# Optimization experiments

Hardware: AMD Instinct MI355X
Metric: run time of the kernel (lower is better)

Reference implementation:

```python
import jax, jax.numpy as jnp
import numpy as np

N_BUS = 4096
BATCH = 1024


def setup_inputs() -> dict:
    key = jax.random.key(0)
    ks = jax.random.split(key, 10)
    u = jax.random.normal(ks[0], (BATCH, N_BUS), dtype=jnp.float32)
    w = jax.random.normal(ks[1], (BATCH, N_BUS), dtype=jnp.float32)
    # parameters (torch.rand -> uniform[0,1); Linear init ~ U(-1/sqrt(n), 1/sqrt(n)))
    G = jax.random.uniform(ks[2], (N_BUS, N_BUS), dtype=jnp.float32)
    B = jax.random.uniform(ks[3], (N_BUS, N_BUS), dtype=jnp.float32)
    bias_p = jax.random.uniform(ks[4], (1, N_BUS), dtype=jnp.float32)
    bias_q = jax.random.uniform(ks[5], (1, N_BUS), dtype=jnp.float32)
    lim = 1.0 / np.sqrt(N_BUS)
    Wp = jax.random.uniform(ks[6], (N_BUS, N_BUS), dtype=jnp.float32, minval=-lim, maxval=lim)
    bp = jax.random.uniform(ks[7], (N_BUS,), dtype=jnp.float32, minval=-lim, maxval=lim)
    Wq = jax.random.uniform(ks[8], (N_BUS, N_BUS), dtype=jnp.float32, minval=-lim, maxval=lim)
    bq = jax.random.uniform(ks[9], (N_BUS,), dtype=jnp.float32, minval=-lim, maxval=lim)
    return {"u": u, "w": w, "G": G, "B": B, "bias_p": bias_p, "bias_q": bias_q,
            "Wp": Wp, "bp": bp, "Wq": Wq, "bq": bq}


def reference(u, w, G, B, bias_p, bias_q, Wp, bp, Wq, bq):
    # Algebraically identical to the original's outer-product form:
    # p_i = sum_k (u_i u_k + w_i w_k) G_ik + (w_i u_k - u_i w_k) B_ik
    #     = u_i (G u)_i + w_i (G w)_i + w_i (B u)_i - u_i (B w)_i
    # q_i = sum_k (w_i u_k - u_i w_k) G_ik - (u_i u_k + w_i w_k) B_ik
    #     = w_i (G u)_i - u_i (G w)_i - u_i (B u)_i - w_i (B w)_i
    Gu = u @ G.T  # (batch, n_bus): (G u)_i = sum_k G_ik u_k
    Gw = w @ G.T
    Bu = u @ B.T
    Bw = w @ B.T
    p = u * Gu + w * Gw + w * Bu - u * Bw + bias_p
    q = w * Gu - u * Gw - u * Bu - w * Bw + bias_q
    # nn.Linear: y = x @ W^T + b
    p = p @ Wp.T + bp
    q = q @ Wq.T + bq
    return (p, q)
```

## Files before the change

kernel.cpp:

```cpp
#include <hip/hip_runtime.h>
#include <hip/hip_bf16.h>

#define NB 4096
#define MB 1024
#define SZ ((size_t)MB * NB)
#define NN ((size_t)NB * NB)

typedef __bf16 bf16_t;
typedef __attribute__((ext_vector_type(8))) __bf16 bf16x8;
typedef __attribute__((ext_vector_type(4))) float f32x4;
typedef __attribute__((ext_vector_type(4))) unsigned int u32x4;

#define AS1 __attribute__((address_space(1)))
#define AS3 __attribute__((address_space(3)))
#define GLOAD16(gp, lp)                                                        \
  __builtin_amdgcn_global_load_lds((const AS1 unsigned int*)(gp),              \
                                   (AS3 unsigned int*)(lp), 16, 0, 0)
#define SBAR() __builtin_amdgcn_s_barrier()
#define SCHEDB() __builtin_amdgcn_sched_barrier(0)
#define MFMA16(a, b, c) __builtin_amdgcn_mfma_f32_16x16x32_bf16((a), (b), (c), 0, 0, 0)
#define VMCNT4() asm volatile("s_waitcnt vmcnt(4)" ::: "memory")
#define VMCNT0() asm volatile("s_waitcnt vmcnt(0)" ::: "memory")

__device__ __forceinline__ bf16x8 neg8(bf16x8 x) {
  u32x4 t;
  __builtin_memcpy(&t, &x, 16);
  t ^= 0x80008000u;
  bf16x8 y;
  __builtin_memcpy(&y, &t, 16);
  return y;
}

__device__ __forceinline__ bf16x8 cvt8(float4 a, float4 b) {
  bf16x8 v;
  v[0] = (bf16_t)a.x; v[1] = (bf16_t)a.y; v[2] = (bf16_t)a.z; v[3] = (bf16_t)a.w;
  v[4] = (bf16_t)b.x; v[5] = (bf16_t)b.y; v[6] = (bf16_t)b.z; v[7] = (bf16_t)b.w;
  return v;
}

#define ITEM_S (SZ / 8)
#define ITEM_N (NN / 8)

__global__ __launch_bounds__(256) void prep6_kernel(
    const float* __restrict__ u, const float* __restrict__ w,
    const float* __restrict__ G, const float* __restrict__ Bm,
    const float* __restrict__ Wp, const float* __restrict__ Wq,
    bf16_t* __restrict__ ws) {
  size_t stride = (size_t)gridDim.x * blockDim.x;
  const size_t tot = 2 * ITEM_S + 4 * ITEM_N;
  for (size_t i = (size_t)blockIdx.x * blockDim.x + threadIdx.x; i < tot;
       i += stride) {
    const float* src;
    bf16_t* dst;
    size_t off;
    if (i < ITEM_S) { src = u; dst = ws; off = i; }
    else if (i < 2 * ITEM_S) { src = w; dst = ws + SZ; off = i - ITEM_S; }
    else if (i < 2 * ITEM_S + ITEM_N) { src = G; dst = ws + 2 * SZ; off = i - 2 * ITEM_S; }
    else if (i < 2 * ITEM_S + 2 * ITEM_N) { src = Bm; dst = ws + 2 * SZ + NN; off = i - 2 * ITEM_S - ITEM_N; }
    else if (i < 2 * ITEM_S + 3 * ITEM_N) { src = Wp; dst = ws + 2 * SZ + 2 * NN; off = i - 2 * ITEM_S - 2 * ITEM_N; }
    else { src = Wq; dst = ws + 2 * SZ + 3 * NN; off = i - 2 * ITEM_S - 3 * ITEM_N; }
    const float4* s = reinterpret_cast<const float4*>(src) + off * 2;
    reinterpret_cast<bf16x8*>(dst)[off] = cvt8(s[0], s[1]);
  }
}

__global__ __launch_bounds__(256) void prep4_kernel(
    const float* __restrict__ u, const float* __restrict__ w,
    const float* __restrict__ G, const float* __restrict__ Bm,
    bf16_t* __restrict__ ws) {
  size_t stride = (size_t)gridDim.x * blockDim.x;
  const size_t tot = 2 * ITEM_S + 2 * ITEM_N;
  for (size_t i = (size_t)blockIdx.x * blockDim.x + threadIdx.x; i < tot;
       i += stride) {
    const float* src;
    bf16_t* dst;
    size_t off;
    if (i < ITEM_S) { src = u; dst = ws; off = i; }
    else if (i < 2 * ITEM_S) { src = w; dst = ws + SZ; off = i - ITEM_S; }
    else if (i < 2 * ITEM_S + ITEM_N) { src = G; dst = ws + 2 * SZ; off = i - 2 * ITEM_S; }
    else { src = Bm; dst = ws + 2 * SZ + NN; off = i - 2 * ITEM_S - ITEM_N; }
    const float4* s = reinterpret_cast<const float4*>(src) + off * 2;
    reinterpret_cast<bf16x8*>(dst)[off] = cvt8(s[0], s[1]);
  }
}

__global__ __launch_bounds__(512, 2) void fused1_v3(
    const float* __restrict__ u, const float* __restrict__ w,
    const bf16_t* __restrict__ ubf, const bf16_t* __restrict__ wbf,
    const bf16_t* __restrict__ Gbf, const bf16_t* __restrict__ Bbf,
    const float* __restrict__ bias_p, const float* __restrict__ bias_q,
    bf16_t* __restrict__ pq) {
  __shared__ bf16_t lds[2][4][128 * 64];
  const int tid = threadIdx.x, lane = tid & 63, wv = tid >> 6;
  const int bid = blockIdx.x;
  const int t = (bid & 7) * 32 + (bid >> 3);
  const int row0 = (t & 7) * 128, col0 = (t >> 3) * 128;
  const int wm = (wv >> 2) * 64, wn = (wv & 3) * 32;
  const int lr = lane & 15, kq = lane >> 4;

  const int rA = tid >> 3;
  const int kkc = (tid & 7) ^ (rA & 7);
  const bf16_t* bases[4] = {ubf, wbf, Gbf, Bbf};
  const int r0s[4] = {row0, row0, col0, col0};
  const bf16_t* gsA[4];
  const bf16_t* gsB[4];
#pragma unroll
  for (int o = 0; o < 4; ++o) {
    gsA[o] = bases[o] + (size_t)(r0s[o] + rA) * NB + kkc * 8;
    gsB[o] = gsA[o] + (size_t)64 * NB;
  }

#define F1_ST(bufv, o, ktn)                                                    \
  do {                                                                         \
    GLOAD16(gsA[o] + (ktn), &lds[bufv][o][wv * 512]);                          \
    GLOAD16(gsB[o] + (ktn), &lds[bufv][o][4096 + wv * 512]);                   \
  } while (0)

  int kread[2], aoff[4], boff[2];
#pragma unroll
  for (int ks = 0; ks < 2; ++ks) kread[ks] = ((ks * 4 + kq) ^ (lr & 7)) << 3;
#pragma unroll
  for (int m = 0; m < 4; ++m) aoff[m] = (wm + m * 16 + lr) * 64;
#pragma unroll
  for (int n = 0; n < 2; ++n) boff[n] = (wn + n * 16 + lr) * 64;

#define F1_LD(o, roff, ks) \
  (*reinterpret_cast<const bf16x8*>(&lds[cur][o][(roff) + kread[ks]]))

  f32x4 aS[4][2] = {}, aT[4][2] = {};

  {
    F1_ST(0, 0, 0); F1_ST(0, 1, 0); F1_ST(0, 2, 0); F1_ST(0, 3, 0);
    VMCNT0();
  }
  __syncthreads();

  const int NIT = NB / 64;
  for (int it = 0; it < NIT; ++it) {
    const int cur = it & 1;
    const int nxt = cur ^ 1;
    const bool pf = (it + 1) < NIT;
    const int ktn = (it + 1) * 64;
#pragma unroll
    for (int ks = 0; ks < 2; ++ks) {
      bf16x8 bG[2], bB[2], bBn[2];
#pragma unroll
      for (int mh = 0; mh < 2; ++mh) {
        if (mh == 0) {
          bG[0] = F1_LD(2, boff[0], ks);
          bG[1] = F1_LD(2, boff[1], ks);
          bB[0] = F1_LD(3, boff[0], ks);
          bB[1] = F1_LD(3, boff[1], ks);
          bBn[0] = neg8(bB[0]);
          bBn[1] = neg8(bB[1]);
        }
        bf16x8 au2[2], aw2[2];
#pragma unroll
        for (int i = 0; i < 2; ++i) {
          au2[i] = F1_LD(0, aoff[2 * mh + i], ks);
          aw2[i] = F1_LD(1, aoff[2 * mh + i], ks);
        }
        if (ks == 0 && pf) {
          if (mh == 0) { F1_ST(nxt, 0, ktn); F1_ST(nxt, 1, ktn); }
          else         { F1_ST(nxt, 2, ktn); F1_ST(nxt, 3, ktn); }
        }
        SBAR();
        SCHEDB();
        __builtin_amdgcn_s_setprio(1);
#pragma unroll
        for (int i = 0; i < 2; ++i) {
          const int m = 2 * mh + i;
#pragma unroll
          for (int n = 0; n < 2; ++n) {
            aS[m][n] = MFMA16(au2[i], bG[n], aS[m][n]);
            aS[m][n] = MFMA16(aw2[i], bBn[n], aS[m][n]);
            aT[m][n] = MFMA16(aw2[i], bG[n], aT[m][n]);
            aT[m][n] = MFMA16(au2[i], bB[n], aT[m][n]);
          }
        }
        __builtin_amdgcn_s_setprio(0);
        SCHEDB();
        if (ks == 1 && mh == 1) VMCNT0();
        SBAR();
        SCHEDB();
      }
    }
  }

  const int fr = lane & 15, fq = kq;
#pragma unroll
  for (int m = 0; m < 4; ++m)
#pragma unroll
    for (int n = 0; n < 2; ++n)
#pragma unroll
      for (int j = 0; j < 4; ++j) {
        int r = row0 + wm + m * 16 + fq * 4 + j;
        int c = col0 + wn + n * 16 + fr;
        size_t idx = (size_t)r * NB + c;
        float U = u[idx], W = w[idx];
        float S = aS[m][n][j], T = aT[m][n][j];
        pq[idx] = (bf16_t)(U * S + W * T + bias_p[c]);
        pq[SZ + idx] = (bf16_t)(W * S - U * T + bias_q[c]);
      }
}

__global__ __launch_bounds__(256, 2) void gemm2_v9(
    const bf16_t* __restrict__ pq, const bf16_t* __restrict__ Wpb,
    const bf16_t* __restrict__ Wqb, const float* __restrict__ bp,
    const float* __restrict__ bq, float* __restrict__ out) {
  __shared__ bf16_t lds[4][2][128 * 32];
  const int tid = threadIdx.x, lane = tid & 63, wv = tid >> 6;
  const int bid = blockIdx.x;
  const int t = (bid & 7) * 64 + (bid >> 3);
  const int z = t >> 8;
  const int s = t & 255;
  const int row0 = (s & 7) * 128, col0 = (s >> 3) * 128;

  const bf16_t* A = pq + (size_t)z * SZ;
  const bf16_t* Wm = z ? Wqb : Wpb;
  const float* bias = z ? bq : bp;
  float* C = out + (size_t)z * SZ;

  const int wm = (wv >> 1) * 64, wn = (wv & 1) * 64;
  const int lr = lane & 15, kq = lane >> 4;
  const int kswz = (kq ^ ((lr >> 1) & 3)) << 3;

  const int srow = tid >> 2;
  const int sc = (tid & 3) ^ ((tid >> 3) & 3);
  const bf16_t* gA0 = A + (size_t)(row0 + srow) * NB + sc * 8;
  const bf16_t* gA1 = gA0 + (size_t)64 * NB;
  const bf16_t* gW0 = Wm + (size_t)(col0 + srow) * NB + sc * 8;
  const bf16_t* gW1 = gW0 + (size_t)64 * NB;

#define G2_ISSUE(hh)                                                           \
  do {                                                                         \
    const int _sl = (hh) & 3;                                                  \
    const int _ko = (hh) * 32;                                                 \
    GLOAD16(gA0 + _ko, &lds[_sl][0][wv * 512]);                                \
    GLOAD16(gA1 + _ko, &lds[_sl][0][2048 + wv * 512]);                         \
    GLOAD16(gW0 + _ko, &lds[_sl][1][wv * 512]);                                \
    GLOAD16(gW1 + _ko, &lds[_sl][1][2048 + wv * 512]);                         \
  } while (0)

  int aoff[4], woff[4];
#pragma unroll
  for (int m = 0; m < 4; ++m) aoff[m] = (wm + m * 16 + lr) * 32 + kswz;
#pragma unroll
  for (int n = 0; n < 4; ++n) woff[n] = (wn + n * 16 + lr) * 32 + kswz;

  f32x4 acc[4][4] = {};

  G2_ISSUE(0); G2_ISSUE(1); G2_ISSUE(2);
  VMCNT4();
  SBAR();
  SCHEDB();

  const int HTOT = 2 * (NB / 64);
  for (int h = 0; h < HTOT; ++h) {
    const int slot = h & 3;
    const bool pf = (h + 3) < HTOT;

    bf16x8 av[4], bw[4];
#pragma unroll
    for (int m = 0; m < 4; ++m)
      av[m] = *reinterpret_cast<const bf16x8*>(&lds[slot][0][aoff[m]]);
#pragma unroll
    for (int n = 0; n < 4; ++n)
      bw[n] = *reinterpret_cast<const bf16x8*>(&lds[slot][1][woff[n]]);
    if (pf) G2_ISSUE(h + 3);
#pragma unroll
    for (int m = 0; m < 4; ++m)
#pragma unroll
      for (int n = 0; n < 4; ++n)
        acc[m][n] = MFMA16(av[m], bw[n], acc[m][n]);
    if (h < HTOT - 3)
      VMCNT4();
    else if (h == HTOT - 3)
      asm volatile("s_waitcnt vmcnt(2)" ::: "memory");
    else if (h == HTOT - 2)
      VMCNT0();
    SBAR();
    SCHEDB();
  }

  const int fr = lane & 15, fq = kq;
#pragma unroll
  for (int m = 0; m < 4; ++m)
#pragma unroll
    for (int n = 0; n < 4; ++n)
#pragma unroll
      for (int j = 0; j < 4; ++j) {
        int r = row0 + wm + m * 16 + fq * 4 + j;
        int c = col0 + wn + n * 16 + fr;
        C[(size_t)r * NB + c] = acc[m][n][j] + bias[c];
      }
}

__device__ __forceinline__ int swz_off32(int r, int kk) {
  return r * 32 + ((kk ^ ((r >> 1) & 3)) << 3);
}

__device__ __forceinline__ void fb_stage_f32(const float* __restrict__ src,
                                             int row0, int k0, bf16_t* lds, int t) {
  int r = t >> 2, kk = t & 3;
  const float* p = src + (size_t)(row0 + r) * NB + k0 + (kk << 3);
  float4 v0 = *reinterpret_cast<const float4*>(p);
  float4 v1 = *reinterpret_cast<const float4*>(p + 4);
  *reinterpret_cast<bf16x8*>(lds + swz_off32(r, kk)) = cvt8(v0, v1);
}

__global__ __launch_bounds__(256, 2) void fb_gemm2(
    const bf16_t* __restrict__ pq, const float* __restrict__ Wp,
    const float* __restrict__ Wq, const float* __restrict__ bp,
    const float* __restrict__ bq, float* __restrict__ out) {
  __shared__ bf16_t lA[128 * 32], lW[128 * 32];
  const int z = blockIdx.z;
  const bf16_t* A = pq + (size_t)z * SZ;
  const float* Wm = z ? Wq : Wp;
  const float* bias = z ? bq : bp;
  float* C = out + (size_t)z * SZ;
  const int tid = threadIdx.x;
  const int lane = tid & 63, wv = tid >> 6;
  const int wm = (wv >> 1) * 64, wn = (wv & 1) * 64;
  const int row0 = blockIdx.y * 128, col0 = blockIdx.x * 128;
  const int lr = lane & 15, kq = lane >> 4;
  const int fslot = (kq ^ ((lr >> 1) & 3)) << 3;
  f32x4 acc[4][4] = {};
  for (int kt = 0; kt < NB; kt += 32) {
#pragma unroll
    for (int p = 0; p < 2; ++p) {
      int cb = p * 256 + wv * 64;
      int ci = cb + lane;
      int r = ci >> 2, kl = ci & 3;
      int ks = kl ^ ((r >> 1) & 3);
      const bf16_t* g = A + (size_t)(row0 + r) * NB + kt + (ks << 3);
      GLOAD16(g, lA + cb * 8);
    }
#pragma unroll
    for (int p = 0; p < 2; ++p)
      fb_stage_f32(Wm, col0, kt, lW, p * 256 + tid);
    __syncthreads();
    bf16x8 af[4], bg[4];
#pragma unroll
    for (int m = 0; m < 4; ++m)
      af[m] = *reinterpret_cast<const bf16x8*>(lA + (wm + m * 16 + lr) * 32 + fslot);
#pragma unroll
    for (int n = 0; n < 4; ++n)
      bg[n] = *reinterpret_cast<const bf16x8*>(lW + (wn + n * 16 + lr) * 32 + fslot);
#pragma unroll
    for (int m = 0; m < 4; ++m)
#pragma unroll
      for (int n = 0; n < 4; ++n)
        acc[m][n] = MFMA16(af[m], bg[n], acc[m][n]);
    __syncthreads();
  }
  const int fr = lane & 15, fq = lane >> 4;
#pragma unroll
  for (int m = 0; m < 4; ++m)
#pragma unroll
    for (int n = 0; n < 4; ++n)
#pragma unroll
      for (int j = 0; j < 4; ++j) {
        int r = row0 + wm + m * 16 + fq * 4 + j;
        int c = col0 + wn + n * 16 + fr;
        C[(size_t)r * NB + c] = acc[m][n][j] + bias[c];
      }
}

__global__ __launch_bounds__(512, 2) void fb_fused1(
    const float* __restrict__ u, const float* __restrict__ w,
    const float* __restrict__ G, const float* __restrict__ Bm,
    const float* __restrict__ bias_p, const float* __restrict__ bias_q,
    bf16_t* __restrict__ pq) {
  __shared__ bf16_t lU[128 * 32], lW[128 * 32], lG[128 * 32], lB[128 * 32];
  const int tid = threadIdx.x;
  const int lane = tid & 63, wv = tid >> 6;
  const int wm = (wv >> 2) * 64, wn = (wv & 3) * 32;
  const int row0 = blockIdx.y * 128, col0 = blockIdx.x * 128;
  const int lr = lane & 15, kq = lane >> 4;
  const int fslot = (kq ^ ((lr >> 1) & 3)) << 3;
  f32x4 aS[4][2] = {}, aT[4][2] = {};
  for (int kt = 0; kt < NB; kt += 32) {
    fb_stage_f32(u, row0, kt, lU, tid);
    fb_stage_f32(w, row0, kt, lW, tid);
    fb_stage_f32(G, col0, kt, lG, tid);
    fb_stage_f32(Bm, col0, kt, lB, tid);
    __syncthreads();
    bf16x8 au[4], aw[4], bG[2], bB[2], bBn[2];
#pragma unroll
    for (int m = 0; m < 4; ++m) {
      int off = (wm + m * 16 + lr) * 32 + fslot;
      au[m] = *reinterpret_cast<const bf16x8*>(lU + off);
      aw[m] = *reinterpret_cast<const bf16x8*>(lW + off);
    }
#pragma unroll
    for (int n = 0; n < 2; ++n) {
      int off = (wn + n * 16 + lr) * 32 + fslot;
      bG[n] = *reinterpret_cast<const bf16x8*>(lG + off);
      bB[n] = *reinterpret_cast<const bf16x8*>(lB + off);
      bBn[n] = neg8(bB[n]);
    }
#pragma unroll
    for (int m = 0; m < 4; ++m)
#pragma unroll
      for (int n = 0; n < 2; ++n) {
        aS[m][n] = MFMA16(au[m], bG[n], aS[m][n]);
        aS[m][n] = MFMA16(aw[m], bBn[n], aS[m][n]);
        aT[m][n] = MFMA16(aw[m], bG[n], aT[m][n]);
        aT[m][n] = MFMA16(au[m], bB[n], aT[m][n]);
      }
    __syncthreads();
  }
  const int fr = lane & 15, fq = lane >> 4;
#pragma unroll
  for (int m = 0; m < 4; ++m)
#pragma unroll
    for (int n = 0; n < 2; ++n)
#pragma unroll
      for (int j = 0; j < 4; ++j) {
        int r = row0 + wm + m * 16 + fq * 4 + j;
        int c = col0 + wn + n * 16 + fr;
        size_t idx = (size_t)r * NB + c;
        float U = u[idx], W = w[idx];
        float S = aS[m][n][j], T = aT[m][n][j];
        pq[idx] = (bf16_t)(U * S + W * T + bias_p[c]);
        pq[SZ + idx] = (bf16_t)(W * S - U * T + bias_q[c]);
      }
}

extern "C" void kernel_launch(void* const* d_in, const int* in_sizes, int n_in,
                              void* d_out, int out_size, void* d_ws, size_t ws_size,
                              hipStream_t stream) {
  const float* u = (const float*)d_in[0];
  const float* w = (const float*)d_in[1];
  const float* G = (const float*)d_in[2];
  const float* Bm = (const float*)d_in[3];
  const float* bias_p = (const float*)d_in[4];
  const float* bias_q = (const float*)d_in[5];
  const float* Wp = (const float*)d_in[6];
  const float* bp = (const float*)d_in[7];
  const float* Wq = (const float*)d_in[8];
  const float* bq = (const float*)d_in[9];
  (void)in_sizes; (void)n_in; (void)out_size;

  const size_t need_full = (6 * SZ + 4 * NN) * sizeof(bf16_t);
  const size_t need_mid = (6 * SZ + 2 * NN) * sizeof(bf16_t);

  if (ws_size >= need_full) {
    bf16_t* ws = (bf16_t*)d_ws;
    bf16_t* ubf = ws;
    bf16_t* wbf = ws + SZ;
    bf16_t* Gbf = ws + 2 * SZ;
    bf16_t* Bbf = Gbf + NN;
    bf16_t* Wpb = Bbf + NN;
    bf16_t* Wqb = Wpb + NN;
    bf16_t* pqw = Wqb + NN;
    prep6_kernel<<<2048, 256, 0, stream>>>(u, w, G, Bm, Wp, Wq, ws);
    fused1_v3<<<256, 512, 0, stream>>>(u, w, ubf, wbf, Gbf, Bbf,
                                       bias_p, bias_q, pqw);
    gemm2_v9<<<512, 256, 0, stream>>>(pqw, Wpb, Wqb, bp, bq, (float*)d_out);
  } else if (ws_size >= need_mid) {
    bf16_t* ws = (bf16_t*)d_ws;
    bf16_t* ubf = ws;
    bf16_t* wbf = ws + SZ;
    bf16_t* Gbf = ws + 2 * SZ;
    bf16_t* Bbf = Gbf + NN;
    bf16_t* pqw = Bbf + NN;
    prep4_kernel<<<2048, 256, 0, stream>>>(u, w, G, Bm, ws);
    fused1_v3<<<256, 512, 0, stream>>>(u, w, ubf, wbf, Gbf, Bbf,
                                       bias_p, bias_q, pqw);
    fb_gemm2<<<dim3(NB / 128, MB / 128, 2), 256, 0, stream>>>(
        pqw, Wp, Wq, bp, bq, (float*)d_out);
  } else {
    bf16_t* pqw = (bf16_t*)d_ws;
    fb_fused1<<<dim3(NB / 128, MB / 128), 512, 0, stream>>>(
        u, w, G, Bm, bias_p, bias_q, pqw);
    fb_gemm2<<<dim3(NB / 128, MB / 128, 2), 256, 0, stream>>>(
        pqw, Wp, Wq, bp, bq, (float*)d_out);
  }
}
```

Baseline: 302.5 us.

## Restructure fused first GEMM to 4-wave 64x64 warp tiles with K-staggered loads

Rewrites the first fused kernel to use 256 threads (4 waves) each computing a 64x64 sub-tile with K-step 32, double-buffered LDS, and a simpler one-barrier-per-step loop. Each wave now holds twice the accumulators and reuses each loaded fragment across more MFMAs, cutting LDS reads per MFMA. Both GEMM kernels also start their K loop at an offset depending on block parity, which spreads concurrent global reads across different addresses. The trade-off is higher register pressure, fewer waves per CU to hide latency, and more barriers per unit of work because the K step is halved.

```diff
diff --git a/kernel.cpp b/kernel.cpp
--- a/kernel.cpp
+++ b/kernel.cpp
@@ -21,6 +21,7 @@
 #define MFMA16(a, b, c) __builtin_amdgcn_mfma_f32_16x16x32_bf16((a), (b), (c), 0, 0, 0)
 #define VMCNT4() asm volatile("s_waitcnt vmcnt(4)" ::: "memory")
 #define VMCNT0() asm volatile("s_waitcnt vmcnt(0)" ::: "memory")
+
 
 __device__ __forceinline__ bf16x8 neg8(bf16x8 x) {
   u32x4 t;
@@ -84,106 +85,87 @@
   }
 }
 
-__global__ __launch_bounds__(512, 2) void fused1_v3(
+__global__ __launch_bounds__(256, 2) void fused1_v9(
     const float* __restrict__ u, const float* __restrict__ w,
     const bf16_t* __restrict__ ubf, const bf16_t* __restrict__ wbf,
     const bf16_t* __restrict__ Gbf, const bf16_t* __restrict__ Bbf,
     const float* __restrict__ bias_p, const float* __restrict__ bias_q,
     bf16_t* __restrict__ pq) {
-  __shared__ bf16_t lds[2][4][128 * 64];
+  __shared__ bf16_t lds[2][4][128 * 32];
   const int tid = threadIdx.x, lane = tid & 63, wv = tid >> 6;
   const int bid = blockIdx.x;
   const int t = (bid & 7) * 32 + (bid >> 3);
   const int row0 = (t & 7) * 128, col0 = (t >> 3) * 128;
-  const int wm = (wv >> 2) * 64, wn = (wv & 3) * 32;
+  const int koff = (bid & 1) << 6;
+  const int wm = (wv >> 1) * 64, wn = (wv & 1) * 64;
   const int lr = lane & 15, kq = lane >> 4;
-
-  const int rA = tid >> 3;
-  const int kkc = (tid & 7) ^ (rA & 7);
-  const bf16_t* bases[4] = {ubf, wbf, Gbf, Bbf};
-  const int r0s[4] = {row0, row0, col0, col0};
+  const int kswz = (kq ^ ((lr >> 1) & 3)) << 3;
+
+  const int srow = tid >> 2;
+  const int sc = (tid & 3) ^ ((tid >> 3) & 3);
   const bf16_t* gsA[4];
   const bf16_t* gsB[4];
-#pragma unroll
-  for (int o = 0; o < 4; ++o) {
-    gsA[o] = bases[o] + (size_t)(r0s[o] + rA) * NB + kkc * 8;
-    gsB[o] = gsA[o] + (size_t)64 * NB;
-  }
-
-#define F1_ST(bufv, o, ktn)                                                    \
-  do {                                                                         \
-    GLOAD16(gsA[o] + (ktn), &lds[bufv][o][wv * 512]);                          \
-    GLOAD16(gsB[o] + (ktn), &lds[bufv][o][4096 + wv * 512]);                   \
+  {
+    const bf16_t* bases[4] = {ubf, wbf, Gbf, Bbf};
+    const int r0s[4] = {row0, row0, col0, col0};
+#pragma unroll
+    for (int o = 0; o < 4; ++o) {
+      gsA[o] = bases[o] + (size_t)(r0s[o] + srow) * NB + sc * 8;
+      gsB[o] = gsA[o] + (size_t)64 * NB;
+    }
+  }
+
+#define F1_ISSUE(hh)                                                          \
+  do {                                                                        \
+    const int _sl = (hh) & 1;                                                 \
+    const int _ko = (((hh) + koff) & 127) * 32;                               \
+    _Pragma("unroll") for (int _o = 0; _o < 4; ++_o) {                        \
+      GLOAD16(gsA[_o] + _ko, &lds[_sl][_o][wv * 512]);                        \
+      GLOAD16(gsB[_o] + _ko, &lds[_sl][_o][2048 + wv * 512]);                 \
+    }                                                                         \
   } while (0)
 
-  int kread[2], aoff[4], boff[2];
-#pragma unroll
-  for (int ks = 0; ks < 2; ++ks) kread[ks] = ((ks * 4 + kq) ^ (lr & 7)) << 3;
-#pragma unroll
-  for (int m = 0; m < 4; ++m) aoff[m] = (wm + m * 16 + lr) * 64;
-#pragma unroll
-  for (int n = 0; n < 2; ++n) boff[n] = (wn + n * 16 + lr) * 64;
-
-#define F1_LD(o, roff, ks) \
-  (*reinterpret_cast<const bf16x8*>(&lds[cur][o][(roff) + kread[ks]]))
-
-  f32x4 aS[4][2] = {}, aT[4][2] = {};
-
-  {
-    F1_ST(0, 0, 0); F1_ST(0, 1, 0); F1_ST(0, 2, 0); F1_ST(0, 3, 0);
-    VMCNT0();
-  }
+  int aoff[4], boff[4];
+#pragma unroll
+  for (int m = 0; m < 4; ++m) aoff[m] = (wm + m * 16 + lr) * 32 + kswz;
+#pragma unroll
+  for (int n = 0; n < 4; ++n) boff[n] = (wn + n * 16 + lr) * 32 + kswz;
+
+  f32x4 aS[4][4] = {}, aT[4][4] = {};
+
+  F1_ISSUE(0);
+  VMCNT0();
   __syncthreads();
 
-  const int NIT = NB / 64;
-  for (int it = 0; it < NIT; ++it) {
-    const int cur = it & 1;
-    const int nxt = cur ^ 1;
-    const bool pf = (it + 1) < NIT;
-    const int ktn = (it + 1) * 64;
-#pragma unroll
-    for (int ks = 0; ks < 2; ++ks) {
-      bf16x8 bG[2], bB[2], bBn[2];
-#pragma unroll
-      for (int mh = 0; mh < 2; ++mh) {
-        if (mh == 0) {
-          bG[0] = F1_LD(2, boff[0], ks);
-          bG[1] = F1_LD(2, boff[1], ks);
-          bB[0] = F1_LD(3, boff[0], ks);
-          bB[1] = F1_LD(3, boff[1], ks);
-          bBn[0] = neg8(bB[0]);
-          bBn[1] = neg8(bB[1]);
-        }
-        bf16x8 au2[2], aw2[2];
-#pragma unroll
-        for (int i = 0; i < 2; ++i) {
-          au2[i] = F1_LD(0, aoff[2 * mh + i], ks);
-          aw2[i] = F1_LD(1, aoff[2 * mh + i], ks);
-        }
-        if (ks == 0 && pf) {
-          if (mh == 0) { F1_ST(nxt, 0, ktn); F1_ST(nxt, 1, ktn); }
-          else         { F1_ST(nxt, 2, ktn); F1_ST(nxt, 3, ktn); }
-        }
-        SBAR();
-        SCHEDB();
-        __builtin_amdgcn_s_setprio(1);
-#pragma unroll
-        for (int i = 0; i < 2; ++i) {
-          const int m = 2 * mh + i;
-#pragma unroll
-          for (int n = 0; n < 2; ++n) {
-            aS[m][n] = MFMA16(au2[i], bG[n], aS[m][n]);
-            aS[m][n] = MFMA16(aw2[i], bBn[n], aS[m][n]);
-            aT[m][n] = MFMA16(aw2[i], bG[n], aT[m][n]);
-            aT[m][n] = MFMA16(au2[i], bB[n], aT[m][n]);
-          }
-        }
-        __builtin_amdgcn_s_setprio(0);
-        SCHEDB();
-        if (ks == 1 && mh == 1) VMCNT0();
-        SBAR();
-        SCHEDB();
-      }
+  for (int h = 0; h < 128; ++h) {
+    const int slot = h & 1;
+    bf16x8 au[4], aw[4], bG[4], bB[4];
+#pragma unroll
+    for (int m = 0; m < 4; ++m) {
+      au[m] = *reinterpret_cast<const bf16x8*>(&lds[slot][0][aoff[m]]);
+      aw[m] = *reinterpret_cast<const bf16x8*>(&lds[slot][1][aoff[m]]);
+    }
+#pragma unroll
+    for (int n = 0; n < 4; ++n) {
+      bG[n] = *reinterpret_cast<const bf16x8*>(&lds[slot][2][boff[n]]);
+      bB[n] = *reinterpret_cast<const bf16x8*>(&lds[slot][3][boff[n]]);
+    }
+    if (h + 1 < 128) F1_ISSUE(h + 1);
+#pragma unroll
+    for (int n = 0; n < 4; ++n) {
+      bf16x8 bn = neg8(bB[n]);
+#pragma unroll
+      for (int m = 0; m < 4; ++m) {
+        aS[m][n] = MFMA16(au[m], bG[n], aS[m][n]);
+        aS[m][n] = MFMA16(aw[m], bn, aS[m][n]);
+        aT[m][n] = MFMA16(aw[m], bG[n], aT[m][n]);
+        aT[m][n] = MFMA16(au[m], bB[n], aT[m][n]);
+      }
+    }
+    if (h + 1 < 128) {
+      VMCNT0();
+      SBAR();
+      SCHEDB();
     }
   }
 
@@ -191,7 +173,7 @@
 #pragma unroll
   for (int m = 0; m < 4; ++m)
 #pragma unroll
-    for (int n = 0; n < 2; ++n)
+    for (int n = 0; n < 4; ++n)
 #pragma unroll
       for (int j = 0; j < 4; ++j) {
         int r = row0 + wm + m * 16 + fq * 4 + j;
@@ -215,6 +197,7 @@
   const int z = t >> 8;
   const int s = t & 255;
   const int row0 = (s & 7) * 128, col0 = (s >> 3) * 128;
+  const int koff = (bid & 1) << 6;
 
   const bf16_t* A = pq + (size_t)z * SZ;
   const bf16_t* Wm = z ? Wqb : Wpb;
@@ -235,7 +218,7 @@
 #define G2_ISSUE(hh)                                                           \
   do {                                                                         \
     const int _sl = (hh) & 3;                                                  \
-    const int _ko = (hh) * 32;                                                 \
+    const int _ko = (((hh) + koff) & 127) * 32;                                \
     GLOAD16(gA0 + _ko, &lds[_sl][0][wv * 512]);                                \
     GLOAD16(gA1 + _ko, &lds[_sl][0][2048 + wv * 512]);                         \
     GLOAD16(gW0 + _ko, &lds[_sl][1][wv * 512]);                                \
@@ -456,7 +439,7 @@
     bf16_t* Wqb = Wpb + NN;
     bf16_t* pqw = Wqb + NN;
     prep6_kernel<<<2048, 256, 0, stream>>>(u, w, G, Bm, Wp, Wq, ws);
-    fused1_v3<<<256, 512, 0, stream>>>(u, w, ubf, wbf, Gbf, Bbf,
+    fused1_v9<<<256, 256, 0, stream>>>(u, w, ubf, wbf, Gbf, Bbf,
                                        bias_p, bias_q, pqw);
     gemm2_v9<<<512, 256, 0, stream>>>(pqw, Wpb, Wqb, bp, bq, (float*)d_out);
   } else if (ws_size >= need_mid) {
@@ -467,7 +450,7 @@
     bf16_t* Bbf = Gbf + NN;
     bf16_t* pqw = Bbf + NN;
     prep4_kernel<<<2048, 256, 0, stream>>>(u, w, G, Bm, ws);
-    fused1_v3<<<256, 512, 0, stream>>>(u, w, ubf, wbf, Gbf, Bbf,
+    fused1_v9<<<256, 256, 0, stream>>>(u, w, ubf, wbf, Gbf, Bbf,
                                        bias_p, bias_q, pqw);
     fb_gemm2<<<dim3(NB / 128, MB / 128, 2), 256, 0, stream>>>(
         pqw, Wp, Wq, bp, bq, (float*)d_out);
```

After: 367.0 us. +21.3%, slower.
